# Kernel tuning notes

Hardware: AMD Instinct MI355X
Metric: run time of the kernel (lower is better)

The kernel has to match this reference:

```python
import jax, jax.numpy as jnp
import numpy as np

N_NODES = 50000
N_EDGES = 500000
H = 128          # h_dim
HEADS = 3
B = 512          # histories with non-zero length
L = 10           # seq_len (all histories full length)
N_RELS = 200
NEG_SLOPE = 0.2  # DGL GATConv default negative_slope


def setup_inputs() -> dict:
    key = jax.random.key(0)
    ks = jax.random.split(key, 18)
    p = lambda i, shape: jax.random.normal(ks[i], shape, jnp.float32) * 0.05
    return {
        "node_feat": jax.random.normal(ks[0], (N_NODES, H), jnp.float32),
        "W1": p(1, (H, HEADS * H)),
        "attn_l1": p(2, (HEADS, H)),
        "attn_r1": p(3, (HEADS, H)),
        "b1": p(4, (HEADS * H,)),
        "W2": p(5, (H, HEADS * H)),
        "attn_l2": p(6, (HEADS, H)),
        "attn_r2": p(7, (HEADS, H)),
        "b2": p(8, (HEADS * H,)),
        "ent_embeds": jax.random.normal(ks[9], (N_NODES, H), jnp.float32),
        "rel_embeds": jax.random.normal(ks[10], (N_RELS, H), jnp.float32),
        "global_emb_list": jax.random.normal(ks[11], (B * L, H), jnp.float32),
        "s_hist_t": jax.random.uniform(ks[12], (B, L), jnp.float32),
        "edge_src": jax.random.randint(ks[13], (N_EDGES,), 0, N_NODES),
        "edge_dst": jax.random.randint(ks[14], (N_EDGES,), 0, N_NODES),
        "node_ids_graph": jax.random.randint(ks[15], (B * L,), 0, N_NODES),
        "s_tem": jax.random.randint(ks[16], (B,), 0, N_NODES),
        "r_tem": jax.random.randint(ks[17], (B,), 0, N_RELS),
    }


def gat_conv(x, W, attn_l, attn_r, bias, src, dst):
    """DGL-style GATConv (allow_zero_in_degree=True, eval mode)."""
    n = x.shape[0]
    feat = (x @ W).reshape(n, HEADS, H)                    # [N, heads, H]
    el = jnp.einsum('nhd,hd->nh', feat, attn_l)            # [N, heads]
    er = jnp.einsum('nhd,hd->nh', feat, attn_r)
    e = jax.nn.leaky_relu(el[src] + er[dst], NEG_SLOPE)    # [E, heads]
    # edge softmax over incoming edges of each dst node
    emax = jax.ops.segment_max(e, dst, num_segments=n)
    ex = jnp.exp(e - emax[dst])
    denom = jax.ops.segment_sum(ex, dst, num_segments=n)
    alpha = ex / denom[dst]                                # [E, heads]
    msg = alpha[:, :, None] * feat[src]                    # [E, heads, H]
    rst = jax.ops.segment_sum(msg, dst, num_segments=n)    # [N, heads, H]
    return rst + bias.reshape(1, HEADS, H)


def reference(node_feat, W1, attn_l1, attn_r1, b1, W2, attn_l2, attn_r2, b2,
              ent_embeds, rel_embeds, global_emb_list, s_hist_t,
              edge_src, edge_dst, node_ids_graph, s_tem, r_tem):
    h = gat_conv(node_feat, W1, attn_l1, attn_r1, b1, edge_src, edge_dst).mean(axis=1)
    h = gat_conv(h, W2, attn_l2, attn_r2, b2, edge_src, edge_dst).mean(axis=1)
    embeds = h[node_ids_graph].reshape(B, L, H)            # gathered history node embeds
    ent = jnp.broadcast_to(ent_embeds[s_tem][:, None, :], (B, L, H))
    rel = jnp.broadcast_to(rel_embeds[r_tem][:, None, :], (B, L, H))
    glob = global_emb_list.reshape(B, L, H)
    seq = jnp.concatenate([embeds, ent, rel, glob], axis=-1)   # [B, L, 4H]
    seq_r = jnp.concatenate([embeds, ent, glob], axis=-1)      # [B, L, 3H]
    return seq, seq_r, s_hist_t
```

## Files before the change

kernel.cpp:

```cpp
#include <hip/hip_runtime.h>
#include <hip/hip_bf16.h>

#define N_NODES 50000
#define N_EDGES 500000
#define HDIM 128
#define HEADS 3
#define BB 512
#define LL 10
#define NEG_SLOPE 0.2f

typedef __hip_bfloat16 bf16;
typedef unsigned char fp8t;
typedef __bf16 v8bf __attribute__((ext_vector_type(8)));
typedef float f32x4 __attribute__((ext_vector_type(4)));


__global__ void k_zero2(int* a, int na, int* b, int nb, int* c){
  int i = blockIdx.x*256 + threadIdx.x;
  if(i < na) a[i] = 0;
  if(i < nb) b[i] = 0;
  if(i == 0) c[0] = 0;
}

__global__ void k_hist(const int* __restrict__ dst, int* __restrict__ cnt, int E){
  int e = blockIdx.x*256 + threadIdx.x;
  if(e < E) atomicAdd(&cnt[dst[e]], 1);
}

__global__ void k_cvt(const float* __restrict__ in, bf16* __restrict__ o, int n){
  int i = (blockIdx.x*256 + threadIdx.x)*8;
  if(i < n){
    f32x4 lo = *reinterpret_cast<const f32x4*>(in + i);
    f32x4 hi = *reinterpret_cast<const f32x4*>(in + i + 4);
    v8bf v;
    #pragma unroll
    for(int j = 0; j < 4; ++j){ v[j] = (__bf16)lo[j]; v[4+j] = (__bf16)hi[j]; }
    *reinterpret_cast<v8bf*>(o + i) = v;
  }
}


#define SCAN_TILE 2048
#define SCAN_NB ((N_NODES + SCAN_TILE - 1)/SCAN_TILE)

__global__ __launch_bounds__(256) void k_scan_part(const int* __restrict__ cnt,
                                                   int* __restrict__ bsum){
  int b = blockIdx.x, tid = threadIdx.x;
  int i0 = b*SCAN_TILE + tid*8;
  int s = 0;
  #pragma unroll
  for(int j = 0; j < 8; ++j){ int i = i0 + j; s += (i < N_NODES) ? cnt[i] : 0; }
  for(int m = 32; m; m >>= 1) s += __shfl_xor(s, m);
  __shared__ int ws[4];
  if((tid & 63) == 0) ws[tid >> 6] = s;
  __syncthreads();
  if(tid == 0) bsum[b] = ws[0] + ws[1] + ws[2] + ws[3];
}

__global__ __launch_bounds__(64) void k_scan_top(int* __restrict__ bsum, int nb){
  int tid = threadIdx.x;
  int v = (tid < nb) ? bsum[tid] : 0;
  for(int s = 1; s < 64; s <<= 1){
    int t = __shfl_up(v, s);
    if(tid >= s) v += t;
  }
  if(tid < nb) bsum[tid] = v;
}

__global__ __launch_bounds__(256) void k_scan_write(int* __restrict__ cnt,
                                                    const int* __restrict__ bsum,
                                                    int* __restrict__ offs){
  int b = blockIdx.x, tid = threadIdx.x;
  int lane = tid & 63, wv = tid >> 6;
  int i0 = b*SCAN_TILE + tid*8;
  int v[8]; int s = 0;
  #pragma unroll
  for(int j = 0; j < 8; ++j){
    int i = i0 + j;
    v[j] = (i < N_NODES) ? cnt[i] : 0;
    s += v[j];
  }
  #pragma unroll
  for(int j = 0; j < 8; ++j){ int i = i0 + j; if(i < N_NODES) cnt[i] = 0; }
  int incl = s;
  for(int sh = 1; sh < 64; sh <<= 1){
    int t = __shfl_up(incl, sh);
    if(lane >= sh) incl += t;
  }
  __shared__ int wtot[4];
  if(lane == 63) wtot[wv] = incl;
  __syncthreads();
  int woff = 0;
  for(int w = 0; w < wv; ++w) woff += wtot[w];
  int excl = woff + incl - s;
  int run = ((b > 0) ? bsum[b-1] : 0) + excl;
  #pragma unroll
  for(int j = 0; j < 8; ++j){
    int i = i0 + j;
    run += v[j];
    if(i < N_NODES) offs[i+1] = run;
  }
  if(b == 0 && tid == 0) offs[0] = 0;
}

__global__ void k_scatter(const int* __restrict__ src, const int* __restrict__ dst,
                          const int* __restrict__ offs, int* __restrict__ cur,
                          int* __restrict__ csr, int E){
  int e = blockIdx.x*256 + threadIdx.x;
  if(e < E){
    int d = dst[e];
    int p = offs[d] + atomicAdd(&cur[d], 1);
    if(p >= 0 && p < E) csr[p] = src[e];
  }
}


__global__ __launch_bounds__(64) void k_mark(const int* __restrict__ nid,
                                             const int* __restrict__ offs,
                                             const int* __restrict__ csr,
                                             unsigned char* __restrict__ mark){
  unsigned n = (unsigned)nid[blockIdx.x];
  if(n >= N_NODES) return;
  if(threadIdx.x == 0) mark[n] = 1;
  int o0 = offs[n], o1 = offs[n+1];
  for(int j = o0 + (int)threadIdx.x; j < o1; j += 64){
    unsigned s = (unsigned)csr[j];
    if(s < N_NODES) mark[s] = 1;
  }
}

__global__ void k_mklist(const unsigned char* __restrict__ mark,
                         int* __restrict__ list, int* __restrict__ cnt){
  int i = blockIdx.x*256 + threadIdx.x;
  if(i < N_NODES && mark[i]){
    int p = atomicAdd(cnt, 1);
    list[p] = i;
  }
}


__global__ void k_wt(const float* __restrict__ W, bf16* __restrict__ Wt){
  int i = blockIdx.x*256 + threadIdx.x;
  if(i < HEADS*HDIM*HDIM){
    int n = i >> 7, k = i & 127;
    Wt[i] = __float2bfloat16(W[k*(HEADS*HDIM) + n]);
  }
}


template<int LIST>
__global__ __launch_bounds__(256) void k_gemm(const bf16* __restrict__ A,
                                              const bf16* __restrict__ Wt,
                                              const float* __restrict__ al,
                                              const float* __restrict__ ar,
                                              fp8t* __restrict__ feat8,
                                              float* __restrict__ el4,
                                              float* __restrict__ er4,
                                              const int* __restrict__ list,
                                              const int* __restrict__ pcnt,
                                              int M){
  int Meff = LIST ? pcnt[0] : M;
  if(blockIdx.x*64 >= Meff) return;
  int tid  = threadIdx.x;
  int wave = tid >> 6, lane = tid & 63;
  int wr = wave >> 1, wc = wave & 1;
  int row0 = blockIdx.x*64 + wr*32;
  int col0 = blockIdx.y*128 + wc*64;
  int l15 = lane & 15, lhi = lane >> 4;

  v8bf a[4][2], b[4][4];
  int nodeA[2];
  #pragma unroll
  for(int mi = 0; mi < 2; ++mi){
    int r = row0 + mi*16 + l15;
    if(r >= Meff) r = Meff - 1;
    nodeA[mi] = LIST ? list[r] : r;
  }
  #pragma unroll
  for(int kk = 0; kk < 4; ++kk){
    int kb = kk*32 + lhi*8;
    #pragma unroll
    for(int mi = 0; mi < 2; ++mi)
      a[kk][mi] = *reinterpret_cast<const v8bf*>(A + (size_t)nodeA[mi]*HDIM + kb);
    #pragma unroll
    for(int ni = 0; ni < 4; ++ni){
      int c = col0 + ni*16 + l15;
      b[kk][ni] = *reinterpret_cast<const v8bf*>(Wt + (size_t)c*HDIM + kb);
    }
  }

  f32x4 acc[2][4] = {};
  #pragma unroll
  for(int kk = 0; kk < 4; ++kk)
    #pragma unroll
    for(int mi = 0; mi < 2; ++mi)
      #pragma unroll
      for(int ni = 0; ni < 4; ++ni)
        acc[mi][ni] = __builtin_amdgcn_mfma_f32_16x16x32_bf16(a[kk][mi], b[kk][ni],
                                                              acc[mi][ni], 0, 0, 0);

  const float* alh = al + blockIdx.y*HDIM;
  const float* arh = ar + blockIdx.y*HDIM;
  float alv[4], arv[4];
  #pragma unroll
  for(int ni = 0; ni < 4; ++ni){
    int d = wc*64 + ni*16 + l15;
    alv[ni] = alh[d]; arv[ni] = arh[d];
  }
  __shared__ float red[2][64][2];
  __shared__ int4 tile4[512];
  fp8t* tile8 = (fp8t*)tile4;

  #pragma unroll
  for(int mi = 0; mi < 2; ++mi){
    #pragma unroll
    for(int j = 0; j < 4; ++j){
      float pe = 0.f, pr = 0.f;
      #pragma unroll
      for(int ni = 0; ni < 4; ++ni){
        pe += acc[mi][ni][j]*alv[ni];
        pr += acc[mi][ni][j]*arv[ni];
      }
      for(int k = 8; k; k >>= 1){ pe += __shfl_xor(pe, k); pr += __shfl_xor(pr, k); }
      int row_l = wr*32 + mi*16 + lhi*4 + j;
      if(l15 == 0){ red[wc][row_l][0] = pe; red[wc][row_l][1] = pr; }
    }
  }
  #pragma unroll
  for(int mi = 0; mi < 2; ++mi)
    #pragma unroll
    for(int j = 0; j < 4; ++j){
      int row_l = wr*32 + mi*16 + lhi*4 + j;
      #pragma unroll
      for(int ni = 0; ni < 4; ++ni){
        float x = acc[mi][ni][j];
        unsigned bb = (unsigned)__builtin_amdgcn_cvt_pk_fp8_f32(x, x, 0, false) & 0xFFu;
        tile8[row_l*128 + wc*64 + ni*16 + l15] = (fp8t)bb;
      }
    }
  __syncthreads();

  if(tid < 64){
    int r = blockIdx.x*64 + tid;
    if(r < Meff){
      int node = LIST ? list[r] : r;
      el4[(size_t)node*4 + blockIdx.y] = red[0][tid][0] + red[1][tid][0];
      er4[(size_t)node*4 + blockIdx.y] = red[0][tid][1] + red[1][tid][1];
    }
  }
  #pragma unroll
  for(int pass = 0; pass < 2; ++pass){
    int off = pass*4096 + tid*16;
    int row_l = off >> 7, col = off & 127;
    int r = blockIdx.x*64 + row_l;
    if(r < Meff){
      int node = LIST ? list[r] : r;
      *reinterpret_cast<int4*>(feat8 + (size_t)node*(HEADS*HDIM) + blockIdx.y*HDIM + col) =
          tile4[off >> 4];
    }
  }
}


__device__ __forceinline__ float lrelu(float x){ return x > 0.f ? x : NEG_SLOPE*x; }

#define SEQ_SZ   (BB*LL*4*HDIM)
#define SEQR_OFF SEQ_SZ
#define SEQR_SZ  (BB*LL*3*HDIM)
#define SH_OFF   (SEQ_SZ + SEQR_SZ)

template<int USE_LIST, int FUSED, int USE_MARK>
__global__ __launch_bounds__(256) void k_agg(const fp8t* __restrict__ feat8,
                                             const float* __restrict__ el4,
                                             const float* __restrict__ er4,
                                             const float* __restrict__ bias,
                                             const int* __restrict__ offs,
                                             const int* __restrict__ csr,
                                             const int* __restrict__ list,
                                             const unsigned char* __restrict__ mark,
                                             bf16* __restrict__ h1,
                                             const float* __restrict__ ent_e,
                                             const float* __restrict__ rel_e,
                                             const float* __restrict__ glob,
                                             const float* __restrict__ sht,
                                             const int* __restrict__ s_tem,
                                             const int* __restrict__ r_tem,
                                             float* __restrict__ out,
                                             int total){
  int widx = blockIdx.x*4 + (threadIdx.x >> 6);
  int lane = threadIdx.x & 63;
  if(widx >= total) return;
  int n = USE_LIST ? list[widx] : widx;
  if(USE_MARK){ if(!mark[n]) return; }
  int o0 = offs[n];
  int deg = offs[n+1] - o0;
  if(deg < 0 || deg > N_EDGES) deg = 0;
  float4 erv = *reinterpret_cast<const float4*>(er4 + (size_t)n*4);

  float aA0=0.f,aA1=0.f,aA2=0.f,aA3=0.f, dhA=0.f;
  float aB0=0.f,aB1=0.f,aB2=0.f,aB3=0.f, dhB=0.f;
  int headA = lane >> 5;

  for(int base = 0; base < deg; base += 64){
    int cn = min(64, deg - base);
    float e0 = 0.f, e1 = 0.f, e2 = 0.f; int s = 0;
    if(lane < cn){
      unsigned su = (unsigned)csr[o0 + base + lane];
      if(su >= N_NODES) su = 0;
      s = (int)su;
      float4 elv = *reinterpret_cast<const float4*>(el4 + (size_t)su*4);
      e0 = __expf(lrelu(elv.x + erv.x));
      e1 = __expf(lrelu(elv.y + erv.y));
      e2 = __expf(lrelu(elv.z + erv.z));
    }
    for(int i = 0; i < cn; ++i){
      int  si = __shfl(s,  i);
      float b0 = __shfl(e0, i);
      float b1 = __shfl(e1, i);
      float b2 = __shfl(e2, i);
      const fp8t* fr = feat8 + (size_t)si*(HEADS*HDIM);
      unsigned uA = *reinterpret_cast<const unsigned*>(fr + lane*4);
      float alA = headA ? b1 : b0;
      dhA += alA;
      aA0 += alA*__builtin_amdgcn_cvt_f32_fp8((int)uA, 0);
      aA1 += alA*__builtin_amdgcn_cvt_f32_fp8((int)uA, 1);
      aA2 += alA*__builtin_amdgcn_cvt_f32_fp8((int)uA, 2);
      aA3 += alA*__builtin_amdgcn_cvt_f32_fp8((int)uA, 3);
      if(lane < 32){
        unsigned uB = *reinterpret_cast<const unsigned*>(fr + 256 + lane*4);
        dhB += b2;
        aB0 += b2*__builtin_amdgcn_cvt_f32_fp8((int)uB, 0);
        aB1 += b2*__builtin_amdgcn_cvt_f32_fp8((int)uB, 1);
        aB2 += b2*__builtin_amdgcn_cvt_f32_fp8((int)uB, 2);
        aB3 += b2*__builtin_amdgcn_cvt_f32_fp8((int)uB, 3);
      }
    }
  }

  float invA = (dhA > 0.f) ? 1.f/dhA : 0.f;
  float invB = (dhB > 0.f) ? 1.f/dhB : 0.f;
  float nA0 = aA0*invA, nA1 = aA1*invA, nA2 = aA2*invA, nA3 = aA3*invA;
  float x0 = __shfl(nA0, lane + 32);
  float x1 = __shfl(nA1, lane + 32);
  float x2 = __shfl(nA2, lane + 32);
  float x3 = __shfl(nA3, lane + 32);
  if(lane < 32){
    int m = lane;
    float4 bs0 = *reinterpret_cast<const float4*>(bias + 4*m);
    float4 bs1 = *reinterpret_cast<const float4*>(bias + HDIM + 4*m);
    float4 bs2 = *reinterpret_cast<const float4*>(bias + 2*HDIM + 4*m);
    float4 r;
    r.x = (nA0 + x0 + aB0*invB + bs0.x + bs1.x + bs2.x)*(1.f/3.f);
    r.y = (nA1 + x1 + aB1*invB + bs0.y + bs1.y + bs2.y)*(1.f/3.f);
    r.z = (nA2 + x2 + aB2*invB + bs0.z + bs1.z + bs2.z)*(1.f/3.f);
    r.w = (nA3 + x3 + aB3*invB + bs0.w + bs1.w + bs2.w)*(1.f/3.f);
    if(FUSED){
      int p = widx, bb = p/LL;
      float4 ent = *reinterpret_cast<const float4*>(ent_e + (size_t)s_tem[bb]*HDIM + 4*m);
      float4 rel = *reinterpret_cast<const float4*>(rel_e + (size_t)r_tem[bb]*HDIM + 4*m);
      float4 gl  = *reinterpret_cast<const float4*>(glob + (size_t)p*HDIM + 4*m);
      float* so = out + (size_t)p*(4*HDIM) + 4*m;
      *reinterpret_cast<float4*>(so)            = r;
      *reinterpret_cast<float4*>(so + HDIM)     = ent;
      *reinterpret_cast<float4*>(so + 2*HDIM)   = rel;
      *reinterpret_cast<float4*>(so + 3*HDIM)   = gl;
      float* ro = out + SEQR_OFF + (size_t)p*(3*HDIM) + 4*m;
      *reinterpret_cast<float4*>(ro)            = r;
      *reinterpret_cast<float4*>(ro + HDIM)     = ent;
      *reinterpret_cast<float4*>(ro + 2*HDIM)   = gl;
      if(m == 0) out[SH_OFF + p] = sht[p];
    } else {
      bf16 t0 = __float2bfloat16(r.x), t1 = __float2bfloat16(r.y);
      bf16 t2 = __float2bfloat16(r.z), t3 = __float2bfloat16(r.w);
      ushort4 hv;
      hv.x = *reinterpret_cast<unsigned short*>(&t0);
      hv.y = *reinterpret_cast<unsigned short*>(&t1);
      hv.z = *reinterpret_cast<unsigned short*>(&t2);
      hv.w = *reinterpret_cast<unsigned short*>(&t3);
      *reinterpret_cast<ushort4*>(h1 + (size_t)n*HDIM + 4*m) = hv;
    }
  }
}


extern "C" void kernel_launch(void* const* d_in, const int* in_sizes, int n_in,
                              void* d_out, int out_size, void* d_ws, size_t ws_size,
                              hipStream_t stream){
  const float* node_feat = (const float*)d_in[0];
  const float* W1        = (const float*)d_in[1];
  const float* attn_l1   = (const float*)d_in[2];
  const float* attn_r1   = (const float*)d_in[3];
  const float* b1        = (const float*)d_in[4];
  const float* W2        = (const float*)d_in[5];
  const float* attn_l2   = (const float*)d_in[6];
  const float* attn_r2   = (const float*)d_in[7];
  const float* b2        = (const float*)d_in[8];
  const float* ent_emb   = (const float*)d_in[9];
  const float* rel_emb   = (const float*)d_in[10];
  const float* glob      = (const float*)d_in[11];
  const float* sht       = (const float*)d_in[12];
  const int*  e_src      = (const int*)d_in[13];
  const int*  e_dst      = (const int*)d_in[14];
  const int*  nid        = (const int*)d_in[15];
  const int*  s_tem      = (const int*)d_in[16];
  const int*  r_tem      = (const int*)d_in[17];
  float* out = (float*)d_out;

  char* ws = (char*)d_ws;
  size_t cur_off = 0;
  auto alloc = [&](size_t bytes)->char*{
    char* r = ws + cur_off;
    cur_off += (bytes + 255) & ~(size_t)255;
    return r;
  };
  fp8t*  feat8 = (fp8t*) alloc((size_t)N_NODES*HEADS*HDIM);
  bf16*  nfb   = (bf16*) alloc((size_t)N_NODES*HDIM*2);
  bf16*  h1    = (bf16*) alloc((size_t)N_NODES*HDIM*2);
  float* el4   = (float*)alloc((size_t)N_NODES*4*4);
  float* er4   = (float*)alloc((size_t)N_NODES*4*4);
  bf16*  wt1   = (bf16*) alloc((size_t)HEADS*HDIM*HDIM*2);
  bf16*  wt2   = (bf16*) alloc((size_t)HEADS*HDIM*HDIM*2);
  int*   offs  = (int*)  alloc((size_t)(N_NODES+1)*4);
  int*   cnt   = (int*)  alloc((size_t)N_NODES*4);
  int*   bsum  = (int*)  alloc((size_t)SCAN_NB*4);
  unsigned char* mark = (unsigned char*)alloc((size_t)N_NODES);
  int*   mlist = (int*)  alloc((size_t)N_NODES*4);
  int*   mcnt  = (int*)  alloc(256);
  int*   csr   = (int*)  alloc((size_t)N_EDGES*4);

  k_zero2<<<(N_NODES+255)/256, 256, 0, stream>>>(cnt, N_NODES,
                                                 (int*)mark, (N_NODES+3)/4, mcnt);
  k_hist<<<(N_EDGES+255)/256, 256, 0, stream>>>(e_dst, cnt, N_EDGES);
  k_scan_part<<<SCAN_NB, 256, 0, stream>>>(cnt, bsum);
  k_scan_top<<<1, 64, 0, stream>>>(bsum, SCAN_NB);
  k_scan_write<<<SCAN_NB, 256, 0, stream>>>(cnt, bsum, offs);
  k_scatter<<<(N_EDGES+255)/256, 256, 0, stream>>>(e_src, e_dst, offs, cnt, csr, N_EDGES);
  k_mark<<<BB*LL, 64, 0, stream>>>(nid, offs, csr, mark);
  k_mklist<<<(N_NODES+255)/256, 256, 0, stream>>>(mark, mlist, mcnt);

  k_wt<<<(HEADS*HDIM*HDIM+255)/256, 256, 0, stream>>>(W1, wt1);
  k_wt<<<(HEADS*HDIM*HDIM+255)/256, 256, 0, stream>>>(W2, wt2);
  k_cvt<<<(N_NODES*HDIM/8+255)/256, 256, 0, stream>>>(node_feat, nfb, N_NODES*HDIM);

  dim3 ggrid((N_NODES + 63)/64, HEADS);

  k_gemm<0><<<ggrid, 256, 0, stream>>>(nfb, wt1, attn_l1, attn_r1,
                                       feat8, el4, er4, nullptr, nullptr, N_NODES);
  k_agg<0,0,1><<<(N_NODES+3)/4, 256, 0, stream>>>(feat8, el4, er4, b1, offs, csr,
                                                  nullptr, mark, h1,
                                                  nullptr, nullptr, nullptr, nullptr,
                                                  nullptr, nullptr, nullptr, N_NODES);

  k_gemm<1><<<ggrid, 256, 0, stream>>>(h1, wt2, attn_l2, attn_r2,
                                       feat8, el4, er4, mlist, mcnt, N_NODES);
  k_agg<1,1,0><<<(BB*LL+3)/4, 256, 0, stream>>>(feat8, el4, er4, b2, offs, csr,
                                                nid, nullptr, nullptr,
                                                ent_emb, rel_emb, glob, sht,
                                                s_tem, r_tem, out, BB*LL);
}
```

Measured before the change: 210.0 us.

## Fuse marking with list build, unroll edge aggregation by four, merge weight transposes

The mark kernel now sets bits atomically and appends each newly marked node straight to the compact list, which removes the separate list-building pass. Layer-one aggregation walks that compact list with 64-thread blocks instead of scanning every node and testing the mark. The per-edge loop no longer broadcasts with shuffles: every lane reads the CSR indices and el values itself, unrolled four edges at a time, so more gathers are in flight. The two weight-transpose launches become one. The trade-offs are redundant index loads in every lane, atomic contention on the list counter, and a layer-one launch sized to all nodes even though most blocks exit early.

```diff
diff --git a/kernel.cpp b/kernel.cpp
--- a/kernel.cpp
+++ b/kernel.cpp
@@ -118,32 +118,31 @@
 __global__ __launch_bounds__(64) void k_mark(const int* __restrict__ nid,
                                              const int* __restrict__ offs,
                                              const int* __restrict__ csr,
-                                             unsigned char* __restrict__ mark){
+                                             unsigned* __restrict__ bits,
+                                             int* __restrict__ list,
+                                             int* __restrict__ cnt){
   unsigned n = (unsigned)nid[blockIdx.x];
   if(n >= N_NODES) return;
-  if(threadIdx.x == 0) mark[n] = 1;
   int o0 = offs[n], o1 = offs[n+1];
-  for(int j = o0 + (int)threadIdx.x; j < o1; j += 64){
-    unsigned s = (unsigned)csr[j];
-    if(s < N_NODES) mark[s] = 1;
-  }
-}
-
-__global__ void k_mklist(const unsigned char* __restrict__ mark,
-                         int* __restrict__ list, int* __restrict__ cnt){
-  int i = blockIdx.x*256 + threadIdx.x;
-  if(i < N_NODES && mark[i]){
-    int p = atomicAdd(cnt, 1);
-    list[p] = i;
-  }
-}
-
-
-__global__ void k_wt(const float* __restrict__ W, bf16* __restrict__ Wt){
+  for(int j = o0 + (int)threadIdx.x - 1; j < o1; j += 64){
+    unsigned s = (j < o0) ? n : (unsigned)csr[j];
+    if(s >= N_NODES) continue;
+    unsigned old = atomicOr(&bits[s >> 5], 1u << (s & 31));
+    if(!((old >> (s & 31)) & 1u)){
+      int p = atomicAdd(cnt, 1);
+      list[p] = (int)s;
+    }
+  }
+}
+
+
+__global__ void k_wt2(const float* __restrict__ W1, const float* __restrict__ W2,
+                      bf16* __restrict__ wt1, bf16* __restrict__ wt2){
   int i = blockIdx.x*256 + threadIdx.x;
   if(i < HEADS*HDIM*HDIM){
     int n = i >> 7, k = i & 127;
-    Wt[i] = __float2bfloat16(W[k*(HEADS*HDIM) + n]);
+    wt1[i] = __float2bfloat16(W1[k*(HEADS*HDIM) + n]);
+    wt2[i] = __float2bfloat16(W2[k*(HEADS*HDIM) + n]);
   }
 }
 
@@ -165,7 +164,8 @@
   int wave = tid >> 6, lane = tid & 63;
   int wr = wave >> 1, wc = wave & 1;
   int row0 = blockIdx.x*64 + wr*32;
-  int col0 = blockIdx.y*128 + wc*64;
+  int head = blockIdx.y;
+  int col0 = head*128 + wc*64;
   int l15 = lane & 15, lhi = lane >> 4;
 
   v8bf a[4][2], b[4][4];
@@ -199,8 +199,8 @@
         acc[mi][ni] = __builtin_amdgcn_mfma_f32_16x16x32_bf16(a[kk][mi], b[kk][ni],
                                                               acc[mi][ni], 0, 0, 0);
 
-  const float* alh = al + blockIdx.y*HDIM;
-  const float* arh = ar + blockIdx.y*HDIM;
+  const float* alh = al + head*HDIM;
+  const float* arh = ar + head*HDIM;
   float alv[4], arv[4];
   #pragma unroll
   for(int ni = 0; ni < 4; ++ni){
@@ -244,8 +244,8 @@
     int r = blockIdx.x*64 + tid;
     if(r < Meff){
       int node = LIST ? list[r] : r;
-      el4[(size_t)node*4 + blockIdx.y] = red[0][tid][0] + red[1][tid][0];
-      er4[(size_t)node*4 + blockIdx.y] = red[0][tid][1] + red[1][tid][1];
+      el4[(size_t)node*4 + head] = red[0][tid][0] + red[1][tid][0];
+      er4[(size_t)node*4 + head] = red[0][tid][1] + red[1][tid][1];
     }
   }
   #pragma unroll
@@ -255,7 +255,7 @@
     int r = blockIdx.x*64 + row_l;
     if(r < Meff){
       int node = LIST ? list[r] : r;
-      *reinterpret_cast<int4*>(feat8 + (size_t)node*(HEADS*HDIM) + blockIdx.y*HDIM + col) =
+      *reinterpret_cast<int4*>(feat8 + (size_t)node*(HEADS*HDIM) + head*HDIM + col) =
           tile4[off >> 4];
     }
   }
@@ -263,111 +263,148 @@
 
 
 __device__ __forceinline__ float lrelu(float x){ return x > 0.f ? x : NEG_SLOPE*x; }
+template<int SEL>
+__device__ __forceinline__ float cv8(unsigned u){
+  return __builtin_amdgcn_cvt_f32_fp8((int)u, SEL);
+}
 
 #define SEQ_SZ   (BB*LL*4*HDIM)
 #define SEQR_OFF SEQ_SZ
 #define SEQR_SZ  (BB*LL*3*HDIM)
 #define SH_OFF   (SEQ_SZ + SEQR_SZ)
 
-template<int USE_LIST, int FUSED, int USE_MARK>
-__global__ __launch_bounds__(256) void k_agg(const fp8t* __restrict__ feat8,
-                                             const float* __restrict__ el4,
-                                             const float* __restrict__ er4,
-                                             const float* __restrict__ bias,
-                                             const int* __restrict__ offs,
-                                             const int* __restrict__ csr,
-                                             const int* __restrict__ list,
-                                             const unsigned char* __restrict__ mark,
-                                             bf16* __restrict__ h1,
-                                             const float* __restrict__ ent_e,
-                                             const float* __restrict__ rel_e,
-                                             const float* __restrict__ glob,
-                                             const float* __restrict__ sht,
-                                             const int* __restrict__ s_tem,
-                                             const int* __restrict__ r_tem,
-                                             float* __restrict__ out,
-                                             int total){
-  int widx = blockIdx.x*4 + (threadIdx.x >> 6);
-  int lane = threadIdx.x & 63;
-  if(widx >= total) return;
+template<int USE_LIST, int FUSED, int USE_PCNT>
+__global__ __launch_bounds__(64) void k_agg(const fp8t* __restrict__ feat8,
+                                            const float* __restrict__ el4,
+                                            const float* __restrict__ er4,
+                                            const float* __restrict__ bias,
+                                            const int* __restrict__ offs,
+                                            const int* __restrict__ csr,
+                                            const int* __restrict__ list,
+                                            const int* __restrict__ pcnt,
+                                            bf16* __restrict__ h1,
+                                            const float* __restrict__ ent_e,
+                                            const float* __restrict__ rel_e,
+                                            const float* __restrict__ glob,
+                                            const float* __restrict__ sht,
+                                            const int* __restrict__ s_tem,
+                                            const int* __restrict__ r_tem,
+                                            float* __restrict__ out,
+                                            int total){
+  int widx = blockIdx.x;
+  int lane = threadIdx.x;
+  int bound = USE_PCNT ? pcnt[0] : total;
+  if(widx >= bound) return;
   int n = USE_LIST ? list[widx] : widx;
-  if(USE_MARK){ if(!mark[n]) return; }
   int o0 = offs[n];
   int deg = offs[n+1] - o0;
   if(deg < 0 || deg > N_EDGES) deg = 0;
   float4 erv = *reinterpret_cast<const float4*>(er4 + (size_t)n*4);
-
-  float aA0=0.f,aA1=0.f,aA2=0.f,aA3=0.f, dhA=0.f;
-  float aB0=0.f,aB1=0.f,aB2=0.f,aB3=0.f, dhB=0.f;
-  int headA = lane >> 5;
-
-  for(int base = 0; base < deg; base += 64){
-    int cn = min(64, deg - base);
-    float e0 = 0.f, e1 = 0.f, e2 = 0.f; int s = 0;
-    if(lane < cn){
-      unsigned su = (unsigned)csr[o0 + base + lane];
-      if(su >= N_NODES) su = 0;
-      s = (int)su;
-      float4 elv = *reinterpret_cast<const float4*>(el4 + (size_t)su*4);
-      e0 = __expf(lrelu(elv.x + erv.x));
-      e1 = __expf(lrelu(elv.y + erv.y));
-      e2 = __expf(lrelu(elv.z + erv.z));
-    }
-    for(int i = 0; i < cn; ++i){
-      int  si = __shfl(s,  i);
-      float b0 = __shfl(e0, i);
-      float b1 = __shfl(e1, i);
-      float b2 = __shfl(e2, i);
-      const fp8t* fr = feat8 + (size_t)si*(HEADS*HDIM);
-      unsigned uA = *reinterpret_cast<const unsigned*>(fr + lane*4);
-      float alA = headA ? b1 : b0;
-      dhA += alA;
-      aA0 += alA*__builtin_amdgcn_cvt_f32_fp8((int)uA, 0);
-      aA1 += alA*__builtin_amdgcn_cvt_f32_fp8((int)uA, 1);
-      aA2 += alA*__builtin_amdgcn_cvt_f32_fp8((int)uA, 2);
-      aA3 += alA*__builtin_amdgcn_cvt_f32_fp8((int)uA, 3);
-      if(lane < 32){
-        unsigned uB = *reinterpret_cast<const unsigned*>(fr + 256 + lane*4);
-        dhB += b2;
-        aB0 += b2*__builtin_amdgcn_cvt_f32_fp8((int)uB, 0);
-        aB1 += b2*__builtin_amdgcn_cvt_f32_fp8((int)uB, 1);
-        aB2 += b2*__builtin_amdgcn_cvt_f32_fp8((int)uB, 2);
-        aB3 += b2*__builtin_amdgcn_cvt_f32_fp8((int)uB, 3);
-      }
+  int hA = lane >> 5;
+  float erA = hA ? erv.y : erv.x;
+  float er2 = erv.z;
+  bool lo = lane < 32;
+
+  float a0=0.f,a1=0.f,a2=0.f,a3=0.f,dhA=0.f;
+  float b0=0.f,b1=0.f,b2=0.f,b3=0.f,dh2=0.f;
+
+  int e = 0;
+  for(; e + 4 <= deg; e += 4){
+    unsigned s0,s1,s2,s3;
+    { unsigned t=(unsigned)csr[o0+e+0]; s0 = (t<N_NODES)?t:0; }
+    { unsigned t=(unsigned)csr[o0+e+1]; s1 = (t<N_NODES)?t:0; }
+    { unsigned t=(unsigned)csr[o0+e+2]; s2 = (t<N_NODES)?t:0; }
+    { unsigned t=(unsigned)csr[o0+e+3]; s3 = (t<N_NODES)?t:0; }
+    float4 v0 = *reinterpret_cast<const float4*>(el4 + (size_t)s0*4);
+    float4 v1 = *reinterpret_cast<const float4*>(el4 + (size_t)s1*4);
+    float4 v2 = *reinterpret_cast<const float4*>(el4 + (size_t)s2*4);
+    float4 v3 = *reinterpret_cast<const float4*>(el4 + (size_t)s3*4);
+    const fp8t* f0 = feat8 + (size_t)s0*(HEADS*HDIM);
+    const fp8t* f1 = feat8 + (size_t)s1*(HEADS*HDIM);
+    const fp8t* f2 = feat8 + (size_t)s2*(HEADS*HDIM);
+    const fp8t* f3 = feat8 + (size_t)s3*(HEADS*HDIM);
+    unsigned uA0 = *reinterpret_cast<const unsigned*>(f0 + lane*4);
+    unsigned uA1 = *reinterpret_cast<const unsigned*>(f1 + lane*4);
+    unsigned uA2 = *reinterpret_cast<const unsigned*>(f2 + lane*4);
+    unsigned uA3 = *reinterpret_cast<const unsigned*>(f3 + lane*4);
+    unsigned uB0=0,uB1=0,uB2=0,uB3=0;
+    if(lo){
+      uB0 = *reinterpret_cast<const unsigned*>(f0 + 256 + lane*4);
+      uB1 = *reinterpret_cast<const unsigned*>(f1 + 256 + lane*4);
+      uB2 = *reinterpret_cast<const unsigned*>(f2 + 256 + lane*4);
+      uB3 = *reinterpret_cast<const unsigned*>(f3 + 256 + lane*4);
+    }
+    float alA0 = __expf(lrelu((hA ? v0.y : v0.x) + erA));
+    float alA1 = __expf(lrelu((hA ? v1.y : v1.x) + erA));
+    float alA2 = __expf(lrelu((hA ? v2.y : v2.x) + erA));
+    float alA3 = __expf(lrelu((hA ? v3.y : v3.x) + erA));
+    dhA += alA0 + alA1 + alA2 + alA3;
+    a0 += alA0*cv8<0>(uA0) + alA1*cv8<0>(uA1) + alA2*cv8<0>(uA2) + alA3*cv8<0>(uA3);
+    a1 += alA0*cv8<1>(uA0) + alA1*cv8<1>(uA1) + alA2*cv8<1>(uA2) + alA3*cv8<1>(uA3);
+    a2 += alA0*cv8<2>(uA0) + alA1*cv8<2>(uA1) + alA2*cv8<2>(uA2) + alA3*cv8<2>(uA3);
+    a3 += alA0*cv8<3>(uA0) + alA1*cv8<3>(uA1) + alA2*cv8<3>(uA2) + alA3*cv8<3>(uA3);
+    if(lo){
+      float al20 = __expf(lrelu(v0.z + er2));
+      float al21 = __expf(lrelu(v1.z + er2));
+      float al22 = __expf(lrelu(v2.z + er2));
+      float al23 = __expf(lrelu(v3.z + er2));
+      dh2 += al20 + al21 + al22 + al23;
+      b0 += al20*cv8<0>(uB0) + al21*cv8<0>(uB1) + al22*cv8<0>(uB2) + al23*cv8<0>(uB3);
+      b1 += al20*cv8<1>(uB0) + al21*cv8<1>(uB1) + al22*cv8<1>(uB2) + al23*cv8<1>(uB3);
+      b2 += al20*cv8<2>(uB0) + al21*cv8<2>(uB1) + al22*cv8<2>(uB2) + al23*cv8<2>(uB3);
+      b3 += al20*cv8<3>(uB0) + al21*cv8<3>(uB1) + al22*cv8<3>(uB2) + al23*cv8<3>(uB3);
+    }
+  }
+  for(; e < deg; ++e){
+    unsigned t = (unsigned)csr[o0+e];
+    unsigned s = (t < N_NODES) ? t : 0;
+    float4 v = *reinterpret_cast<const float4*>(el4 + (size_t)s*4);
+    const fp8t* fr = feat8 + (size_t)s*(HEADS*HDIM);
+    unsigned uA = *reinterpret_cast<const unsigned*>(fr + lane*4);
+    float alA = __expf(lrelu((hA ? v.y : v.x) + erA));
+    dhA += alA;
+    a0 += alA*cv8<0>(uA); a1 += alA*cv8<1>(uA);
+    a2 += alA*cv8<2>(uA); a3 += alA*cv8<3>(uA);
+    if(lo){
+      unsigned uB = *reinterpret_cast<const unsigned*>(fr + 256 + lane*4);
+      float al2 = __expf(lrelu(v.z + er2));
+      dh2 += al2;
+      b0 += al2*cv8<0>(uB); b1 += al2*cv8<1>(uB);
+      b2 += al2*cv8<2>(uB); b3 += al2*cv8<3>(uB);
     }
   }
 
   float invA = (dhA > 0.f) ? 1.f/dhA : 0.f;
-  float invB = (dhB > 0.f) ? 1.f/dhB : 0.f;
-  float nA0 = aA0*invA, nA1 = aA1*invA, nA2 = aA2*invA, nA3 = aA3*invA;
+  float inv2 = (dh2 > 0.f) ? 1.f/dh2 : 0.f;
+  float nA0 = a0*invA, nA1 = a1*invA, nA2 = a2*invA, nA3 = a3*invA;
   float x0 = __shfl(nA0, lane + 32);
   float x1 = __shfl(nA1, lane + 32);
   float x2 = __shfl(nA2, lane + 32);
   float x3 = __shfl(nA3, lane + 32);
-  if(lane < 32){
+  if(lo){
     int m = lane;
     float4 bs0 = *reinterpret_cast<const float4*>(bias + 4*m);
     float4 bs1 = *reinterpret_cast<const float4*>(bias + HDIM + 4*m);
     float4 bs2 = *reinterpret_cast<const float4*>(bias + 2*HDIM + 4*m);
     float4 r;
-    r.x = (nA0 + x0 + aB0*invB + bs0.x + bs1.x + bs2.x)*(1.f/3.f);
-    r.y = (nA1 + x1 + aB1*invB + bs0.y + bs1.y + bs2.y)*(1.f/3.f);
-    r.z = (nA2 + x2 + aB2*invB + bs0.z + bs1.z + bs2.z)*(1.f/3.f);
-    r.w = (nA3 + x3 + aB3*invB + bs0.w + bs1.w + bs2.w)*(1.f/3.f);
+    r.x = (nA0 + x0 + b0*inv2 + bs0.x + bs1.x + bs2.x)*(1.f/3.f);
+    r.y = (nA1 + x1 + b1*inv2 + bs0.y + bs1.y + bs2.y)*(1.f/3.f);
+    r.z = (nA2 + x2 + b2*inv2 + bs0.z + bs1.z + bs2.z)*(1.f/3.f);
+    r.w = (nA3 + x3 + b3*inv2 + bs0.w + bs1.w + bs2.w)*(1.f/3.f);
     if(FUSED){
       int p = widx, bb = p/LL;
       float4 ent = *reinterpret_cast<const float4*>(ent_e + (size_t)s_tem[bb]*HDIM + 4*m);
       float4 rel = *reinterpret_cast<const float4*>(rel_e + (size_t)r_tem[bb]*HDIM + 4*m);
       float4 gl  = *reinterpret_cast<const float4*>(glob + (size_t)p*HDIM + 4*m);
       float* so = out + (size_t)p*(4*HDIM) + 4*m;
-      *reinterpret_cast<float4*>(so)            = r;
-      *reinterpret_cast<float4*>(so + HDIM)     = ent;
-      *reinterpret_cast<float4*>(so + 2*HDIM)   = rel;
-      *reinterpret_cast<float4*>(so + 3*HDIM)   = gl;
+      *reinterpret_cast<float4*>(so)          = r;
+      *reinterpret_cast<float4*>(so + HDIM)   = ent;
+      *reinterpret_cast<float4*>(so + 2*HDIM) = rel;
+      *reinterpret_cast<float4*>(so + 3*HDIM) = gl;
       float* ro = out + SEQR_OFF + (size_t)p*(3*HDIM) + 4*m;
-      *reinterpret_cast<float4*>(ro)            = r;
-      *reinterpret_cast<float4*>(ro + HDIM)     = ent;
-      *reinterpret_cast<float4*>(ro + 2*HDIM)   = gl;
+      *reinterpret_cast<float4*>(ro)          = r;
+      *reinterpret_cast<float4*>(ro + HDIM)   = ent;
+      *reinterpret_cast<float4*>(ro + 2*HDIM) = gl;
       if(m == 0) out[SH_OFF + p] = sht[p];
     } else {
       bf16 t0 = __float2bfloat16(r.x), t1 = __float2bfloat16(r.y);
@@ -423,38 +460,36 @@
   int*   offs  = (int*)  alloc((size_t)(N_NODES+1)*4);
   int*   cnt   = (int*)  alloc((size_t)N_NODES*4);
   int*   bsum  = (int*)  alloc((size_t)SCAN_NB*4);
-  unsigned char* mark = (unsigned char*)alloc((size_t)N_NODES);
+  unsigned* bits = (unsigned*)alloc(((size_t)N_NODES/32 + 1)*4);
   int*   mlist = (int*)  alloc((size_t)N_NODES*4);
   int*   mcnt  = (int*)  alloc(256);
   int*   csr   = (int*)  alloc((size_t)N_EDGES*4);
 
   k_zero2<<<(N_NODES+255)/256, 256, 0, stream>>>(cnt, N_NODES,
-                                                 (int*)mark, (N_NODES+3)/4, mcnt);
+                                                 (int*)bits, N_NODES/32 + 1, mcnt);
   k_hist<<<(N_EDGES+255)/256, 256, 0, stream>>>(e_dst, cnt, N_EDGES);
   k_scan_part<<<SCAN_NB, 256, 0, stream>>>(cnt, bsum);
   k_scan_top<<<1, 64, 0, stream>>>(bsum, SCAN_NB);
   k_scan_write<<<SCAN_NB, 256, 0, stream>>>(cnt, bsum, offs);
   k_scatter<<<(N_EDGES+255)/256, 256, 0, stream>>>(e_src, e_dst, offs, cnt, csr, N_EDGES);
-  k_mark<<<BB*LL, 64, 0, stream>>>(nid, offs, csr, mark);
-  k_mklist<<<(N_NODES+255)/256, 256, 0, stream>>>(mark, mlist, mcnt);
-
-  k_wt<<<(HEADS*HDIM*HDIM+255)/256, 256, 0, stream>>>(W1, wt1);
-  k_wt<<<(HEADS*HDIM*HDIM+255)/256, 256, 0, stream>>>(W2, wt2);
+  k_mark<<<BB*LL, 64, 0, stream>>>(nid, offs, csr, bits, mlist, mcnt);
+
+  k_wt2<<<(HEADS*HDIM*HDIM+255)/256, 256, 0, stream>>>(W1, W2, wt1, wt2);
   k_cvt<<<(N_NODES*HDIM/8+255)/256, 256, 0, stream>>>(node_feat, nfb, N_NODES*HDIM);
 
   dim3 ggrid((N_NODES + 63)/64, HEADS);
 
   k_gemm<0><<<ggrid, 256, 0, stream>>>(nfb, wt1, attn_l1, attn_r1,
                                        feat8, el4, er4, nullptr, nullptr, N_NODES);
-  k_agg<0,0,1><<<(N_NODES+3)/4, 256, 0, stream>>>(feat8, el4, er4, b1, offs, csr,
-                                                  nullptr, mark, h1,
-                                                  nullptr, nullptr, nullptr, nullptr,
-                                                  nullptr, nullptr, nullptr, N_NODES);
+  k_agg<1,0,1><<<N_NODES, 64, 0, stream>>>(feat8, el4, er4, b1, offs, csr,
+                                           mlist, mcnt, h1,
+                                           nullptr, nullptr, nullptr, nullptr,
+                                           nullptr, nullptr, nullptr, N_NODES);
 
   k_gemm<1><<<ggrid, 256, 0, stream>>>(h1, wt2, attn_l2, attn_r2,
                                        feat8, el4, er4, mlist, mcnt, N_NODES);
-  k_agg<1,1,0><<<(BB*LL+3)/4, 256, 0, stream>>>(feat8, el4, er4, b2, offs, csr,
-                                                nid, nullptr, nullptr,
-                                                ent_emb, rel_emb, glob, sht,
-                                                s_tem, r_tem, out, BB*LL);
-}
+  k_agg<1,1,0><<<BB*LL, 64, 0, stream>>>(feat8, el4, er4, b2, offs, csr,
+                                         nid, nullptr, nullptr,
+                                         ent_emb, rel_emb, glob, sht,
+                                         s_tem, r_tem, out, BB*LL);
+}
```

New measurement: 237.5 us. +13.1%, slower.
